# Kernel optimization log

Hardware: AMD Instinct MI355X
Metric: run time of the kernel (lower is better)

## Reference

```python
import jax, jax.numpy as jnp
import numpy as np

SEQ_LEN = 65536
H = 30   # h_dim_rnn
P = 25   # h_dim_params


def setup_inputs() -> dict:
    key = jax.random.key(0)
    ks = jax.random.split(key, 12)
    sc = 0.1  # modest weight scale for numerical sanity
    return {
        "params": jax.random.normal(ks[0], (1, 11), jnp.float32),
        "seq": jax.random.normal(ks[1], (1, SEQ_LEN), jnp.float32),
        "phi_W": jax.random.normal(ks[2], (P, 11), jnp.float32) * sc,
        "phi_b": jax.random.normal(ks[3], (P,), jnp.float32) * sc,
        "W_ih": jax.random.normal(ks[4], (3 * H, P + 1), jnp.float32) * sc,
        "b_ih": jax.random.normal(ks[5], (3 * H,), jnp.float32) * sc,
        "W_hh": jax.random.normal(ks[6], (3 * H, H), jnp.float32) * sc,
        "b_hh": jax.random.normal(ks[7], (3 * H,), jnp.float32) * sc,
        "head_W1": jax.random.normal(ks[8], (H, H), jnp.float32) * sc,
        "head_b1": jax.random.normal(ks[9], (H,), jnp.float32) * sc,
        "head_W2": jax.random.normal(ks[10], (1, H), jnp.float32) * sc,
        "head_b2": jax.random.normal(ks[11], (1,), jnp.float32) * sc,
    }


def reference(params, seq, phi_W, phi_b, W_ih, b_ih, W_hh, b_hh,
              head_W1, head_b1, head_W2, head_b2):
    # phi: [P] (batch_size is structurally 1 in the original module)
    phi = jax.nn.relu(params @ phi_W.T + phi_b)[0]
    s = seq[0]                       # [S]
    seq_len = s.shape[0]

    def step(h, st):
        s_prev, tgt = st
        x = jnp.concatenate([phi, s_prev[None]])      # [P+1]
        gi = W_ih @ x + b_ih                          # [3H], gate order r,z,n
        gh = W_hh @ h + b_hh                          # [3H]
        r = jax.nn.sigmoid(gi[:H] + gh[:H])
        z = jax.nn.sigmoid(gi[H:2 * H] + gh[H:2 * H])
        n = jnp.tanh(gi[2 * H:] + r * gh[2 * H:])
        h_new = (1.0 - z) * n + z * h
        hid = jax.nn.relu(head_W1 @ h_new + head_b1)  # [H]
        pred = head_W2 @ hid + head_b2                # [1]
        # MSELoss(pred[1,1,1], target[1]) broadcasts -> scalar squared error
        return h_new, (pred[0] - tgt) ** 2

    h0 = jnp.zeros((H,), seq.dtype)
    _, losses = jax.lax.scan(step, h0, (s[:-1], s[1:]))  # t = 1..seq_len-1
    return jnp.sum(losses) / seq_len
```

## Files before the change

### kernel.cpp

```cpp
#include <hip/hip_runtime.h>

#define Hh 30
#define Pp 25
#define SEQN 65536
#define NSTEP 65535
#define HSTRIDE 32
#define CHUNK 64
#define WARM  192
#define NCHUNK (SEQN / CHUNK)

__attribute__((amdgpu_flat_work_group_size(64, 64)))
__attribute__((amdgpu_waves_per_eu(1, 1)))
__global__ void rnn_seq_kernel(
    const float* __restrict__ params, const float* __restrict__ seq,
    const float* __restrict__ phi_W, const float* __restrict__ phi_b,
    const float* __restrict__ W_ih, const float* __restrict__ b_ih,
    const float* __restrict__ W_hh, const float* __restrict__ b_hh,
    float* __restrict__ h_out)
{
    __shared__ float phi_s[Pp];
    __shared__ float c_s[3 * Hh], u_s[3 * Hh];

    const int lane = threadIdx.x;

    if (lane < Pp) {
        float acc = phi_b[lane];
        #pragma unroll
        for (int k = 0; k < 11; ++k) acc = fmaf(params[k], phi_W[lane * 11 + k], acc);
        phi_s[lane] = fmaxf(acc, 0.f);
    }
    __syncthreads();

    for (int j = lane; j < 3 * Hh; j += 64) {
        float acc = b_ih[j];
        #pragma unroll
        for (int p = 0; p < Pp; ++p) acc = fmaf(W_ih[j * (Pp + 1) + p], phi_s[p], acc);
        c_s[j] = acc;
        u_s[j] = W_ih[j * (Pp + 1) + Pp];
    }
    __syncthreads();

    const int half = lane >> 5;
    const int li   = min(lane & 31, Hh - 1);
    const int jb   = half * 15;

    float w_r[15], w_z[15], w_n[15];
    #pragma unroll
    for (int j = 0; j < 15; ++j) {
        w_r[j] = W_hh[li * Hh + jb + j];
        w_z[j] = W_hh[(Hh + li) * Hh + jb + j];
        w_n[j] = W_hh[(2 * Hh + li) * Hh + jb + j];
    }
    #pragma unroll
    for (int j = 0; j < 15; ++j) {
        asm volatile("" : "+v"(w_r[j]), "+v"(w_z[j]), "+v"(w_n[j]));
    }

    const bool  lo  = (half == 0);
    const float crL = lo ? (c_s[li] + b_hh[li]) : 0.f;
    const float czL = lo ? (c_s[Hh + li] + b_hh[Hh + li]) : 0.f;
    const float urL = lo ? u_s[li] : 0.f;
    const float uzL = lo ? u_s[Hh + li] : 0.f;
    const float gnI = lo ? b_hh[2 * Hh + li] : 0.f;
    const float cn  = c_s[2 * Hh + li];
    const float un  = u_s[2 * Hh + li];

    const int hbase = jb << 2;

    const int cL = blockIdx.x * CHUNK;
    const int t0 = (cL >= WARM) ? (cL - WARM) : 0;

    float hn = 0.f;
    float seqv = seq[t0 + lane];
    const int col = (lane < Hh) ? lane : 31;
    float* hptr = h_out + (size_t)cL * HSTRIDE + col;

    for (int tb = t0; tb < cL + CHUNK; tb += 64) {
        float seqnx = seq[min(tb + 64 + lane, SEQN - 1)];
        const bool dostore = (tb >= cL);

        #pragma unroll 4
        for (int k = 0; k < 64; ++k) {
            float sv = __int_as_float(__builtin_amdgcn_readlane(__float_as_int(seqv), k));

            float hv[15];
            #pragma unroll
            for (int j = 0; j < 15; ++j)
                hv[j] = __int_as_float(
                    __builtin_amdgcn_ds_bpermute(hbase + (j << 2), __float_as_int(hn)));

            float ar = fmaf(urL, sv, crL);
            float az = fmaf(uzL, sv, czL);
            float gn = gnI;
            #pragma unroll
            for (int j = 0; j < 15; ++j) {
                ar = fmaf(w_r[j], hv[j], ar);
                az = fmaf(w_z[j], hv[j], az);
                gn = fmaf(w_n[j], hv[j], gn);
            }

            float ar2 = ar, az2 = az, gn2 = gn;
            asm("v_permlane32_swap_b32 %0, %1" : "+v"(ar), "+v"(ar2));
            asm("v_permlane32_swap_b32 %0, %1" : "+v"(az), "+v"(az2));
            asm("v_permlane32_swap_b32 %0, %1" : "+v"(gn), "+v"(gn2));
            ar += ar2; az += az2; gn += gn2;

            float r = __builtin_amdgcn_rcpf(1.f + __expf(-ar));
            float z = __builtin_amdgcn_rcpf(1.f + __expf(-az));
            float bn = fmaf(r, gn, fmaf(un, sv, cn));
            float n  = 1.f - 2.f * __builtin_amdgcn_rcpf(1.f + __expf(2.f * bn));
            hn = fmaf(z, hn - n, n);

            if (dostore) {
                hptr[0] = hn;
                hptr += HSTRIDE;
            }
        }
        seqv = seqnx;
    }
}

__global__ __launch_bounds__(256) void head_kernel(
    const float* __restrict__ h_out, const float* __restrict__ seq,
    const float* __restrict__ head_W1, const float* __restrict__ head_b1,
    const float* __restrict__ head_W2, const float* __restrict__ head_b2,
    float* __restrict__ out)
{
    __shared__ float w1s[Hh * Hh];
    __shared__ float b1s[Hh];
    __shared__ float w2s[Hh];
    const int tid = threadIdx.x;
    for (int i = tid; i < Hh * Hh; i += 256) w1s[i] = head_W1[i];
    if (tid < Hh) { b1s[tid] = head_b1[tid]; w2s[tid] = head_W2[tid]; }
    __syncthreads();

    int t = blockIdx.x * 256 + tid;
    float sq = 0.f;
    if (t < NSTEP) {
        float hv[Hh];
        #pragma unroll
        for (int j = 0; j < Hh; ++j) hv[j] = h_out[t * HSTRIDE + j];
        float pred = head_b2[0];
        for (int kk = 0; kk < Hh; ++kk) {
            float acc = b1s[kk];
            #pragma unroll
            for (int j = 0; j < Hh; ++j) acc = fmaf(w1s[kk * Hh + j], hv[j], acc);
            pred = fmaf(fmaxf(acc, 0.f), w2s[kk], pred);
        }
        float e = pred - seq[t + 1];
        sq = e * e;
    }
    #pragma unroll
    for (int off = 32; off > 0; off >>= 1) sq += __shfl_down(sq, off);
    __shared__ float wsum[4];
    if ((tid & 63) == 0) wsum[tid >> 6] = sq;
    __syncthreads();
    if (tid == 0) {
        float tot = (wsum[0] + wsum[1] + wsum[2] + wsum[3]) * (1.f / 65536.f);
        atomicAdd(out, tot);
    }
}

extern "C" void kernel_launch(void* const* d_in, const int* in_sizes, int n_in,
                              void* d_out, int out_size, void* d_ws, size_t ws_size,
                              hipStream_t stream)
{
    const float* params = (const float*)d_in[0];
    const float* seq    = (const float*)d_in[1];
    const float* phi_W  = (const float*)d_in[2];
    const float* phi_b  = (const float*)d_in[3];
    const float* W_ih   = (const float*)d_in[4];
    const float* b_ih   = (const float*)d_in[5];
    const float* W_hh   = (const float*)d_in[6];
    const float* b_hh   = (const float*)d_in[7];
    const float* hW1    = (const float*)d_in[8];
    const float* hb1    = (const float*)d_in[9];
    const float* hW2    = (const float*)d_in[10];
    const float* hb2    = (const float*)d_in[11];
    float* out  = (float*)d_out;
    float* h_ws = (float*)d_ws;

    hipMemsetAsync(out, 0, sizeof(float), stream);
    rnn_seq_kernel<<<NCHUNK, 64, 0, stream>>>(params, seq, phi_W, phi_b,
                                              W_ih, b_ih, W_hh, b_hh, h_ws);
    head_kernel<<<(NSTEP + 255) / 256, 256, 0, stream>>>(h_ws, seq,
                                                         hW1, hb1, hW2, hb2, out);
}
```

Measured before the change: 169.3 us.

## Fuse MLP head and loss into RNN kernel via LDS hidden-state buffer

Hidden states for each chunk now go to a padded shared-memory buffer (stride 33) instead of a global workspace. The same block then evaluates the MLP head on its 64 rows and atomically accumulates the squared error. This removes the second kernel launch and the global round trip of the hidden states. In exchange, each of the 1024 single-wave blocks does head work serially after its recurrence, and there are 4x more atomics.

```diff
diff --git a/kernel.cpp b/kernel.cpp
--- a/kernel.cpp
+++ b/kernel.cpp
@@ -3,23 +3,27 @@
 #define Hh 30
 #define Pp 25
 #define SEQN 65536
-#define NSTEP 65535
-#define HSTRIDE 32
 #define CHUNK 64
 #define WARM  192
 #define NCHUNK (SEQN / CHUNK)
+#define HST 33
 
 __attribute__((amdgpu_flat_work_group_size(64, 64)))
 __attribute__((amdgpu_waves_per_eu(1, 1)))
-__global__ void rnn_seq_kernel(
+__global__ void rnn_fused_kernel(
     const float* __restrict__ params, const float* __restrict__ seq,
     const float* __restrict__ phi_W, const float* __restrict__ phi_b,
     const float* __restrict__ W_ih, const float* __restrict__ b_ih,
     const float* __restrict__ W_hh, const float* __restrict__ b_hh,
-    float* __restrict__ h_out)
+    const float* __restrict__ head_W1, const float* __restrict__ head_b1,
+    const float* __restrict__ head_W2, const float* __restrict__ head_b2,
+    float* __restrict__ out)
 {
     __shared__ float phi_s[Pp];
     __shared__ float c_s[3 * Hh], u_s[3 * Hh];
+    __shared__ float w1s[Hh * Hh];
+    __shared__ float b1s[Hh], w2s[Hh];
+    __shared__ float hbuf[CHUNK * HST];
 
     const int lane = threadIdx.x;
 
@@ -29,6 +33,8 @@
         for (int k = 0; k < 11; ++k) acc = fmaf(params[k], phi_W[lane * 11 + k], acc);
         phi_s[lane] = fmaxf(acc, 0.f);
     }
+    for (int i = lane; i < Hh * Hh; i += 64) w1s[i] = head_W1[i];
+    if (lane < Hh) { b1s[lane] = head_b1[lane]; w2s[lane] = head_W2[lane]; }
     __syncthreads();
 
     for (int j = lane; j < 3 * Hh; j += 64) {
@@ -73,11 +79,11 @@
     float hn = 0.f;
     float seqv = seq[t0 + lane];
     const int col = (lane < Hh) ? lane : 31;
-    float* hptr = h_out + (size_t)cL * HSTRIDE + col;
 
     for (int tb = t0; tb < cL + CHUNK; tb += 64) {
         float seqnx = seq[min(tb + 64 + lane, SEQN - 1)];
         const bool dostore = (tb >= cL);
+        const int rbase = tb - cL;
 
         #pragma unroll 4
         for (int k = 0; k < 64; ++k) {
@@ -111,54 +117,33 @@
             float n  = 1.f - 2.f * __builtin_amdgcn_rcpf(1.f + __expf(2.f * bn));
             hn = fmaf(z, hn - n, n);
 
-            if (dostore) {
-                hptr[0] = hn;
-                hptr += HSTRIDE;
-            }
+            if (dostore) hbuf[(rbase + k) * HST + col] = hn;
         }
         seqv = seqnx;
     }
-}
-
-__global__ __launch_bounds__(256) void head_kernel(
-    const float* __restrict__ h_out, const float* __restrict__ seq,
-    const float* __restrict__ head_W1, const float* __restrict__ head_b1,
-    const float* __restrict__ head_W2, const float* __restrict__ head_b2,
-    float* __restrict__ out)
-{
-    __shared__ float w1s[Hh * Hh];
-    __shared__ float b1s[Hh];
-    __shared__ float w2s[Hh];
-    const int tid = threadIdx.x;
-    for (int i = tid; i < Hh * Hh; i += 256) w1s[i] = head_W1[i];
-    if (tid < Hh) { b1s[tid] = head_b1[tid]; w2s[tid] = head_W2[tid]; }
     __syncthreads();
 
-    int t = blockIdx.x * 256 + tid;
-    float sq = 0.f;
-    if (t < NSTEP) {
-        float hv[Hh];
+    const int tt = cL + 1 + lane;
+    const float tgt = seq[min(tt, SEQN - 1)];
+    const float b2v = head_b2[0];
+
+    float hrow[Hh];
+    #pragma unroll
+    for (int j = 0; j < Hh; ++j) hrow[j] = hbuf[lane * HST + j];
+
+    float pred = b2v;
+    for (int kk = 0; kk < Hh; ++kk) {
+        float acc = b1s[kk];
         #pragma unroll
-        for (int j = 0; j < Hh; ++j) hv[j] = h_out[t * HSTRIDE + j];
-        float pred = head_b2[0];
-        for (int kk = 0; kk < Hh; ++kk) {
-            float acc = b1s[kk];
-            #pragma unroll
-            for (int j = 0; j < Hh; ++j) acc = fmaf(w1s[kk * Hh + j], hv[j], acc);
-            pred = fmaf(fmaxf(acc, 0.f), w2s[kk], pred);
-        }
-        float e = pred - seq[t + 1];
-        sq = e * e;
+        for (int j = 0; j < Hh; ++j) acc = fmaf(w1s[kk * Hh + j], hrow[j], acc);
+        pred = fmaf(fmaxf(acc, 0.f), w2s[kk], pred);
     }
+    float e = pred - tgt;
+    float sq = (tt < SEQN) ? e * e : 0.f;
+
     #pragma unroll
     for (int off = 32; off > 0; off >>= 1) sq += __shfl_down(sq, off);
-    __shared__ float wsum[4];
-    if ((tid & 63) == 0) wsum[tid >> 6] = sq;
-    __syncthreads();
-    if (tid == 0) {
-        float tot = (wsum[0] + wsum[1] + wsum[2] + wsum[3]) * (1.f / 65536.f);
-        atomicAdd(out, tot);
-    }
+    if (lane == 0) atomicAdd(out, sq * (1.f / 65536.f));
 }
 
 extern "C" void kernel_launch(void* const* d_in, const int* in_sizes, int n_in,
@@ -178,11 +163,9 @@
     const float* hW2    = (const float*)d_in[10];
     const float* hb2    = (const float*)d_in[11];
     float* out  = (float*)d_out;
-    float* h_ws = (float*)d_ws;
 
     hipMemsetAsync(out, 0, sizeof(float), stream);
-    rnn_seq_kernel<<<NCHUNK, 64, 0, stream>>>(params, seq, phi_W, phi_b,
-                                              W_ih, b_ih, W_hh, b_hh, h_ws);
-    head_kernel<<<(NSTEP + 255) / 256, 256, 0, stream>>>(h_ws, seq,
-                                                         hW1, hb1, hW2, hb2, out);
+    rnn_fused_kernel<<<NCHUNK, 64, 0, stream>>>(params, seq, phi_W, phi_b,
+                                                W_ih, b_ih, W_hh, b_hh,
+                                                hW1, hb1, hW2, hb2, out);
 }
```

New measurement: 169.9 us. About the same (+0.3%).
